# Kernel optimization log

Hardware: AMD Instinct MI355X
Metric: run time of the kernel (lower is better)

## Reference

```python
import jax, jax.numpy as jnp
import numpy as np

B, T, E, H, W = 2, 1024, 1024, 8, 31
D = 2 * W + 1  # head dim must equal 2*window_size+1 for the rel-pos broadcast


def _ln(x, w, b):
    mu = jnp.mean(x, axis=-1, keepdims=True)
    var = jnp.mean(jnp.square(x - mu), axis=-1, keepdims=True)
    return (x - mu) * jax.lax.rsqrt(var + 1e-5) * w + b


def setup_inputs() -> dict:
    key = jax.random.key(0)
    k = jax.random.split(key, 8)
    s = 0.02
    return {
        "x": jax.random.normal(k[0], (B, T, E // 2), jnp.float32),
        "ln1_w": jnp.ones(E, jnp.float32), "ln1_b": jnp.zeros(E, jnp.float32),
        "qkv_w": jax.random.normal(k[1], (3 * H * D, E), jnp.float32) * s,
        "qkv_b": jnp.zeros(3 * H * D, jnp.float32),
        "rel_pos": jax.random.normal(k[2], (D, D), jnp.float32) * s,
        "proj_w": jax.random.normal(k[3], (E, H * D), jnp.float32) * s,
        "proj_b": jnp.zeros(E, jnp.float32),
        "ln2_w": jnp.ones(E, jnp.float32), "ln2_b": jnp.zeros(E, jnp.float32),
        "fc_w": jax.random.normal(k[4], (4 * E, E), jnp.float32) * s,
        "fc_b": jnp.zeros(4 * E, jnp.float32),
        "cproj_w": jax.random.normal(k[5], (E, 4 * E), jnp.float32) * s,
        "cproj_b": jnp.zeros(E, jnp.float32),
    }


def reference(x, ln1_w, ln1_b, qkv_w, qkv_b, rel_pos, proj_w, proj_b,
              ln2_w, ln2_b, fc_w, fc_b, cproj_w, cproj_b):
    # --- RotaryEmbedding: angle = x * inv_freq; out = cat(sin, cos) -> [B,T,E]
    dim = 2 * x.shape[-1]
    inv_freq = 1.0 / 10000.0 ** (jnp.arange(0, dim, 2, dtype=jnp.float32) / dim)
    ang = x * inv_freq
    xr = jnp.concatenate([jnp.sin(ang), jnp.cos(ang)], axis=-1)  # [B,T,E]

    # --- custom windowed attention on ln_1(xr)
    h = _ln(xr, ln1_w, ln1_b)
    qkv = h @ qkv_w.T + qkv_b                       # [B,T,3*H*D]
    q, k, v = jnp.split(qkv, 3, axis=-1)

    def heads(t):
        return t.reshape(B, T, H, D).transpose(0, 2, 1, 3)  # [B,H,T,D]

    q, k, v = heads(q), heads(k), heads(v)
    # per-token q-outer-k scores (einsum '...bd,...bv->...bdv'): [B,H,T,D,D]
    scores = jnp.einsum('bhtd,bhtv->bhtdv', q, k)
    # rel-pos bias: Embedding lookup at offsets -W..W (negative indices wrap)
    bias = rel_pos[jnp.arange(-W, W + 1) % D]       # [D, D] == [2W+1, d_model]
    attn = jax.nn.softmax(scores + bias, axis=-2)   # softmax over non-canonical axis
    out = jnp.einsum('bhtdv,bhtv->bhtd', attn, v)   # apply per-token attn matrix to v
    out = out.transpose(0, 2, 1, 3).reshape(B, T, H * D)
    xa = xr + out @ proj_w.T + proj_b               # residual

    # --- MLP
    h2 = _ln(xa, ln2_w, ln2_b)
    m = jax.nn.gelu(h2 @ fc_w.T + fc_b, approximate=False) @ cproj_w.T + cproj_b
    return xa + m
```

## Files before the change

### kernel.cpp

```cpp
#include <hip/hip_runtime.h>
#include <hip/hip_bf16.h>


typedef __bf16 bf16;
typedef bf16 bf16x8 __attribute__((ext_vector_type(8)));
typedef bf16 bf16x4 __attribute__((ext_vector_type(4)));
typedef bf16 bf16x2 __attribute__((ext_vector_type(2)));
typedef float f32x4 __attribute__((ext_vector_type(4)));

__device__ __forceinline__ float rdlane(float x, int l)
{
    return __int_as_float(__builtin_amdgcn_readlane(__float_as_int(x), l));
}

__global__ __launch_bounds__(256) void rotary_ln_kernel(
    const float* __restrict__ x, const float* __restrict__ w,
    const float* __restrict__ b, float* __restrict__ xr, bf16* __restrict__ Y)
{
    const int row = blockIdx.x;
    const int tid = threadIdx.x;
    float2 xv = *(const float2*)(x + (size_t)row * 512 + tid * 2);
    float i0 = exp2f(-(float)(2*tid)     * 0.025952563241307518f);
    float i1 = exp2f(-(float)(2*tid + 1) * 0.025952563241307518f);
    float a0 = xv.x * i0, a1 = xv.y * i1;
    float s0 = sinf(a0), s1 = sinf(a1);
    float c0 = cosf(a0), c1 = cosf(a1);
    *(float2*)(xr + (size_t)row * 1024 + tid*2)       = make_float2(s0, s1);
    *(float2*)(xr + (size_t)row * 1024 + 512 + tid*2) = make_float2(c0, c1);
    float s  = s0 + s1 + c0 + c1;
    float ss = s0*s0 + s1*s1 + c0*c0 + c1*c1;
    #pragma unroll
    for (int off = 32; off > 0; off >>= 1) {
        s  += __shfl_down(s, off);
        ss += __shfl_down(ss, off);
    }
    __shared__ float rs[4], rss[4];
    int wave = tid >> 6, lane = tid & 63;
    if (lane == 0) { rs[wave] = s; rss[wave] = ss; }
    __syncthreads();
    s  = rs[0] + rs[1] + rs[2] + rs[3];
    ss = rss[0] + rss[1] + rss[2] + rss[3];
    float mu   = s * (1.f / 1024.f);
    float var  = ss * (1.f / 1024.f) - mu * mu;
    float rstd = rsqrtf(var + 1e-5f);
    float2 w0 = *(const float2*)(w + tid*2);
    float2 b0 = *(const float2*)(b + tid*2);
    float2 w1 = *(const float2*)(w + 512 + tid*2);
    float2 b1 = *(const float2*)(b + 512 + tid*2);
    bf16x2 y0, y1;
    y0[0] = (bf16)((s0 - mu) * rstd * w0.x + b0.x);
    y0[1] = (bf16)((s1 - mu) * rstd * w0.y + b0.y);
    y1[0] = (bf16)((c0 - mu) * rstd * w1.x + b1.x);
    y1[1] = (bf16)((c1 - mu) * rstd * w1.y + b1.y);
    *(bf16x2*)(Y + (size_t)row * 1024 + tid*2)       = y0;
    *(bf16x2*)(Y + (size_t)row * 1024 + 512 + tid*2) = y1;
}

__device__ __forceinline__ void conv_chunk(
    const float* __restrict__ src, bf16* __restrict__ dst,
    int ci, int N, int K, int Kp)
{
    int kpc = Kp >> 3;
    int r  = ci / kpc;
    int kc = (ci - r * kpc) << 3;
    bf16x8 o;
    if (r < N && kc < K) {
        float4 f0 = *(const float4*)(src + (size_t)r * K + kc);
        float4 f1 = *(const float4*)(src + (size_t)r * K + kc + 4);
        o[0]=(bf16)f0.x; o[1]=(bf16)f0.y; o[2]=(bf16)f0.z; o[3]=(bf16)f0.w;
        o[4]=(bf16)f1.x; o[5]=(bf16)f1.y; o[6]=(bf16)f1.z; o[7]=(bf16)f1.w;
    } else {
        #pragma unroll
        for (int j = 0; j < 8; ++j) o[j] = (bf16)0.f;
    }
    *(bf16x8*)(dst + (size_t)r * Kp + kc) = o;
}

__global__ __launch_bounds__(256) void conv_all_kernel(
    const float* __restrict__ qkv_w, const float* __restrict__ proj_w,
    const float* __restrict__ fc_w,  const float* __restrict__ cproj_w,
    const float* __restrict__ qkv_b,
    bf16* __restrict__ wqkv, bf16* __restrict__ wproj,
    bf16* __restrict__ wfc,  bf16* __restrict__ wcproj,
    float* __restrict__ qkvb_p)
{
    if (blockIdx.x == 5120) {
        for (int i = threadIdx.x; i < 1536; i += 256)
            qkvb_p[i] = (i < 1512) ? qkv_b[i] : 0.f;
        return;
    }
    int idx = blockIdx.x * 256 + threadIdx.x;
    if      (idx < 196608)  conv_chunk(qkv_w,   wqkv,   idx,          1512, 1024, 1024);
    else if (idx < 262144)  conv_chunk(proj_w,  wproj,  idx - 196608, 1024,  504,  512);
    else if (idx < 786432)  conv_chunk(fc_w,    wfc,    idx - 262144, 4096, 1024, 1024);
    else                    conv_chunk(cproj_w, wcproj, idx - 786432, 1024, 4096, 4096);
}

__device__ __forceinline__ void gload16(const char* src, char* ldsdst)
{
    __builtin_amdgcn_global_load_lds(
        (const __attribute__((address_space(1))) void*)src,
        (__attribute__((address_space(3))) void*)ldsdst, 16, 0, 0);
}
__device__ __forceinline__ float gelu_exact(float v)
{
    return 0.5f * v * (1.f + erff(v * 0.70710678118654752f));
}

template<int EPI>
__global__ __launch_bounds__(256, 4) void gemm6_kernel(
    const bf16* __restrict__ A, const bf16* __restrict__ Wt,
    const float* __restrict__ bias, bf16* __restrict__ Cb,
    int N, int Kp, int ksplit)
{
    __shared__ __align__(16) char lds[2][12288];

    const int tid  = threadIdx.x;
    const int w    = tid >> 6;
    const int lane = tid & 63;

    const int gx = gridDim.x, gy = gridDim.y;
    const int nwg = gx * gy * gridDim.z;
    const int chunk = nwg >> 3;
    int id = (blockIdx.z * gy + blockIdx.y) * gx + blockIdx.x;
    int sw = (id & 7) * chunk + (id >> 3);
    const int bx = sw % gx;
    const int t2 = sw / gx;
    const int by = t2 % gy;
    const int bz = t2 / gy;

    const int row0 = by * 64;
    const int col0 = bx * 128;
    const int wr = (w >> 1) * 32;
    const int wc = (w & 1) * 64;
    const int rl = lane & 15;
    const int kb16 = (lane >> 4) * 16;

    const size_t strideBy = (size_t)Kp * 2;
    const size_t kz = (size_t)bz * ksplit * 2;
    const char* Abase = (const char*)A  + (size_t)row0 * strideBy + kz;
    const char* Wbase = (const char*)Wt + (size_t)col0 * strideBy + kz;

    const size_t srcA0 = (size_t)(tid >> 2) * strideBy + (tid & 3) * 16;
    size_t srcB[2];
    #pragma unroll
    for (int i = 0; i < 2; ++i) {
        int o = (i * 256 + tid) * 16;
        srcB[i] = (size_t)(o >> 6) * strideBy + (o & 63);
    }

    f32x4 acc[2][4] = {};

    auto STAGE = [&](int buf, int kt) {
        const char* ab = Abase + (size_t)kt * 64;
        const char* wb = Wbase + (size_t)kt * 64;
        gload16(ab + srcA0, &lds[buf][0] + tid * 16);
        #pragma unroll
        for (int i = 0; i < 2; ++i)
            gload16(wb + srcB[i], &lds[buf][4096] + (i * 256 + tid) * 16);
    };

    const int niter = ksplit >> 5;
    STAGE(0, 0);
    __syncthreads();
    for (int kt = 0; kt < niter; ++kt) {
        if (kt + 1 < niter)
            STAGE((kt + 1) & 1, kt + 1);
        const char* base = lds[kt & 1];
        bf16x8 af[2], bfr[4];
        #pragma unroll
        for (int mi = 0; mi < 2; ++mi)
            af[mi] = *(const bf16x8*)(base + ((wr + mi*16 + rl) << 6) + kb16);
        #pragma unroll
        for (int nj = 0; nj < 4; ++nj)
            bfr[nj] = *(const bf16x8*)(base + 4096 + ((wc + nj*16 + rl) << 6) + kb16);
        __builtin_amdgcn_s_setprio(1);
        #pragma unroll
        for (int mi = 0; mi < 2; ++mi)
            #pragma unroll
            for (int nj = 0; nj < 4; ++nj)
                acc[mi][nj] = __builtin_amdgcn_mfma_f32_16x16x32_bf16(
                    af[mi], bfr[nj], acc[mi][nj], 0, 0, 0);
        __builtin_amdgcn_s_setprio(0);
        __syncthreads();
    }

    const int rq = (lane >> 4) * 4;
    bf16* Cbz = Cb;
    if (EPI == 3) Cbz += (size_t)bz * 2048 * N;
    #pragma unroll
    for (int mi = 0; mi < 2; ++mi) {
        #pragma unroll
        for (int rj = 0; rj < 4; ++rj) {
            int row = row0 + wr + mi*16 + rq + rj;
            #pragma unroll
            for (int nj = 0; nj < 4; ++nj) {
                int col = col0 + wc + nj*16 + rl;
                float c = acc[mi][nj][rj];
                size_t off = (size_t)row * N + col;
                if (EPI == 0)      Cbz[off] = (bf16)(c + bias[col]);
                else if (EPI == 1) Cbz[off] = (bf16)gelu_exact(c + bias[col]);
                else               Cbz[off] = (bf16)c;
            }
        }
    }
}

template<int P>
__global__ __launch_bounds__(256) void reduce_kernel(
    const bf16* __restrict__ parts, const float* __restrict__ bias,
    const float* R, float* out)
{
    int row = blockIdx.x;
    int c = threadIdx.x * 4;
    size_t off = (size_t)row * 1024 + c;
    float4 bv = *(const float4*)(bias + c);
    float4 o = *(const float4*)(R + off);
    o.x += bv.x; o.y += bv.y; o.z += bv.z; o.w += bv.w;
    #pragma unroll
    for (int p = 0; p < P; ++p) {
        bf16x4 v = *(const bf16x4*)(parts + (size_t)p * 2048 * 1024 + off);
        o.x += (float)v[0]; o.y += (float)v[1];
        o.z += (float)v[2]; o.w += (float)v[3];
    }
    *(float4*)(out + off) = o;
}

__global__ __launch_bounds__(256) void reduceln_kernel(
    const bf16* __restrict__ parts, const float* __restrict__ bias,
    const float* __restrict__ R, const float* __restrict__ lnw,
    const float* __restrict__ lnb, float* __restrict__ out,
    bf16* __restrict__ Y)
{
    int row = blockIdx.x;
    int c = threadIdx.x * 4;
    size_t off = (size_t)row * 1024 + c;
    float4 bv = *(const float4*)(bias + c);
    float4 o  = *(const float4*)(R + off);
    o.x += bv.x; o.y += bv.y; o.z += bv.z; o.w += bv.w;
    #pragma unroll
    for (int p = 0; p < 2; ++p) {
        bf16x4 v = *(const bf16x4*)(parts + (size_t)p * 2048 * 1024 + off);
        o.x += (float)v[0]; o.y += (float)v[1];
        o.z += (float)v[2]; o.w += (float)v[3];
    }
    *(float4*)(out + off) = o;
    float s  = o.x + o.y + o.z + o.w;
    float ss = o.x*o.x + o.y*o.y + o.z*o.z + o.w*o.w;
    #pragma unroll
    for (int of = 32; of > 0; of >>= 1) {
        s  += __shfl_down(s, of);
        ss += __shfl_down(ss, of);
    }
    __shared__ float rs[4], rss[4];
    int wave = threadIdx.x >> 6, lane = threadIdx.x & 63;
    if (lane == 0) { rs[wave] = s; rss[wave] = ss; }
    __syncthreads();
    s  = rs[0] + rs[1] + rs[2] + rs[3];
    ss = rss[0] + rss[1] + rss[2] + rss[3];
    float mu  = s * (1.f / 1024.f);
    float var = ss * (1.f / 1024.f) - mu * mu;
    float rstd = rsqrtf(var + 1e-5f);
    float4 wv = *(const float4*)(lnw + c);
    float4 lb = *(const float4*)(lnb + c);
    bf16 y[4];
    y[0] = (bf16)((o.x - mu) * rstd * wv.x + lb.x);
    y[1] = (bf16)((o.y - mu) * rstd * wv.y + lb.y);
    y[2] = (bf16)((o.z - mu) * rstd * wv.z + lb.z);
    y[3] = (bf16)((o.w - mu) * rstd * wv.w + lb.w);
    *(uint2*)(Y + (size_t)row * 1024 + c) = *(uint2*)y;
}

__global__ __launch_bounds__(1024) void attn3_kernel(
    const bf16* __restrict__ qkv, const float* __restrict__ rel_pos,
    bf16* __restrict__ outp)
{
    __shared__ float bR[4096];
    __shared__ float bT[4096];
    for (int i = threadIdx.x; i < 4096; i += 1024) {
        int d = i >> 6, v = i & 63;
        float val = (d < 63 && v < 63)
                  ? rel_pos[((d + 32) % 63) * 63 + v] * 1.4426950408889634f
                  : -1e30f;
        bR[(d << 6) + (((v >> 2) ^ (d & 15)) << 2) + (v & 3)] = val;
        bT[(v << 6) + (((d >> 2) ^ (v & 15)) << 2) + (d & 3)] = val;
    }
    __syncthreads();

    const int wave = threadIdx.x >> 6;
    const int lane = threadIdx.x & 63;
    const int tk  = blockIdx.x * 16 + wave;
    const int row = tk >> 3;
    const int h   = tk & 7;
    const bf16* base = qkv + (size_t)row * 1536 + h * 63;
    float q_own = 0.f, k_own = 0.f, v_own = 0.f;
    if (lane < 63) {
        q_own = (float)base[lane] * 1.4426950408889634f;
        k_own = (float)base[504 + lane];
        v_own = (float)base[1008 + lane];
    }

    const float* myT = bT + (lane << 6);
    const int sw = lane & 15;
    float z0 = 0.f, z1 = 0.f, z2 = 0.f, z3 = 0.f;
    #pragma unroll
    for (int g = 0; g < 16; ++g) {
        f32x4 bb = *(const f32x4*)(myT + ((g ^ sw) << 2));
        z0 += __builtin_amdgcn_exp2f(fmaf(rdlane(q_own, 4*g + 0), k_own, bb[0]));
        z1 += __builtin_amdgcn_exp2f(fmaf(rdlane(q_own, 4*g + 1), k_own, bb[1]));
        z2 += __builtin_amdgcn_exp2f(fmaf(rdlane(q_own, 4*g + 2), k_own, bb[2]));
        z3 += __builtin_amdgcn_exp2f(fmaf(rdlane(q_own, 4*g + 3), k_own, bb[3]));
    }
    float Z = (z0 + z1) + (z2 + z3);
    float w_own = (lane < 63) ? v_own / Z : 0.f;

    const float* myR = bR + (lane << 6);
    float a0 = 0.f, a1 = 0.f, a2 = 0.f, a3 = 0.f;
    #pragma unroll
    for (int g = 0; g < 16; ++g) {
        f32x4 bb = *(const f32x4*)(myR + ((g ^ sw) << 2));
        a0 = fmaf(__builtin_amdgcn_exp2f(fmaf(q_own, rdlane(k_own, 4*g + 0), bb[0])),
                  rdlane(w_own, 4*g + 0), a0);
        a1 = fmaf(__builtin_amdgcn_exp2f(fmaf(q_own, rdlane(k_own, 4*g + 1), bb[1])),
                  rdlane(w_own, 4*g + 1), a1);
        a2 = fmaf(__builtin_amdgcn_exp2f(fmaf(q_own, rdlane(k_own, 4*g + 2), bb[2])),
                  rdlane(w_own, 4*g + 2), a2);
        a3 = fmaf(__builtin_amdgcn_exp2f(fmaf(q_own, rdlane(k_own, 4*g + 3), bb[3])),
                  rdlane(w_own, 4*g + 3), a3);
    }
    float acc = (a0 + a1) + (a2 + a3);

    if (lane < 63)
        outp[(size_t)row * 512 + h*63 + lane] = (bf16)acc;
    if (h == 7 && lane == 63) {
        #pragma unroll
        for (int j = 0; j < 8; ++j)
            outp[(size_t)row * 512 + 504 + j] = (bf16)0.f;
    }
}

extern "C" void kernel_launch(void* const* d_in, const int* in_sizes, int n_in,
                              void* d_out, int out_size, void* d_ws, size_t ws_size,
                              hipStream_t stream)
{
    const float* x       = (const float*)d_in[0];
    const float* ln1_w   = (const float*)d_in[1];
    const float* ln1_b   = (const float*)d_in[2];
    const float* qkv_w   = (const float*)d_in[3];
    const float* qkv_b   = (const float*)d_in[4];
    const float* rel_pos = (const float*)d_in[5];
    const float* proj_w  = (const float*)d_in[6];
    const float* proj_b  = (const float*)d_in[7];
    const float* ln2_w   = (const float*)d_in[8];
    const float* ln2_b   = (const float*)d_in[9];
    const float* fc_w    = (const float*)d_in[10];
    const float* fc_b    = (const float*)d_in[11];
    const float* cproj_w = (const float*)d_in[12];
    const float* cproj_b = (const float*)d_in[13];
    float* out = (float*)d_out;

    char* p = (char*)d_ws;
    float* xr      = (float*)p;            p += (size_t)2048*1024*4;
    bf16*  h_bf    = (bf16*)p;             p += (size_t)2048*1024*2;
    bf16*  wqkv    = (bf16*)p;             p += (size_t)1536*1024*2;
    bf16*  wproj   = (bf16*)p;             p += (size_t)1024*512*2;
    bf16*  wfc     = (bf16*)p;             p += (size_t)4096*1024*2;
    bf16*  wcproj  = (bf16*)p;             p += (size_t)1024*4096*2;
    float* qkvb_p  = (float*)p;            p += 8192;
    bf16*  attn_bf = (bf16*)p;             p += (size_t)2048*512*2;
    bf16*  qkvb    = (bf16*)p;
    bf16*  fc_act  = (bf16*)p;
    bf16*  proj_part = qkvb;
    bf16*  cp_part = (bf16*)d_ws;

    conv_all_kernel<<<5121, 256, 0, stream>>>(qkv_w, proj_w, fc_w, cproj_w, qkv_b,
                                              wqkv, wproj, wfc, wcproj, qkvb_p);
    rotary_ln_kernel<<<2048, 256, 0, stream>>>(x, ln1_w, ln1_b, xr, h_bf);
    gemm6_kernel<0><<<dim3(12,32,1), 256, 0, stream>>>(h_bf, wqkv, qkvb_p,
                                                       qkvb, 1536, 1024, 1024);
    attn3_kernel<<<1024, 1024, 0, stream>>>(qkvb, rel_pos, attn_bf);
    gemm6_kernel<3><<<dim3(8,32,2), 256, 0, stream>>>(attn_bf, wproj, nullptr,
                                                      proj_part, 1024, 512, 256);
    reduceln_kernel<<<2048, 256, 0, stream>>>(proj_part, proj_b, xr,
                                              ln2_w, ln2_b, out, h_bf);
    gemm6_kernel<1><<<dim3(32,32,1), 256, 0, stream>>>(h_bf, wfc, fc_b,
                                                       fc_act, 4096, 1024, 1024);
    gemm6_kernel<3><<<dim3(8,32,4), 256, 0, stream>>>(fc_act, wcproj, nullptr,
                                                      cp_part, 1024, 4096, 1024);
    reduce_kernel<4><<<2048, 256, 0, stream>>>(cp_part, cproj_b, out, out);
}
```

Before: 144.5 us.

## Triple-buffer GEMM LDS staging with XOR swizzle and explicit waitcnt barriers

The GEMM kernel moves from double to triple buffering in LDS, prefetching two K-tiles ahead. __syncthreads is replaced by explicit vmcnt/lgkmcnt waits plus s_barrier, so global-to-LDS loads can stay in flight across iterations. An XOR swizzle on the 16-byte slots of each 64-byte row is applied to both the direct-to-LDS loads and the fragment reads, aimed at reducing LDS bank conflicts. This raises LDS use to 36KB per block, which may limit occupancy at 4 blocks per CU, and the hand-coded wait counts must match the exact number of issued loads.

New measurement: 149.4 us. 1.03x slower.

```diff
diff --git a/kernel.cpp b/kernel.cpp
--- a/kernel.cpp
+++ b/kernel.cpp
@@ -96,6 +96,19 @@
     else                    conv_chunk(cproj_w, wcproj, idx - 786432, 1024, 4096, 4096);
 }
 
+template<int N> __device__ __forceinline__ void vmwait()
+{
+    if constexpr      (N==0) asm volatile("s_waitcnt vmcnt(0)" ::: "memory");
+    else if constexpr (N==3) asm volatile("s_waitcnt vmcnt(3)" ::: "memory");
+}
+__device__ __forceinline__ void lgkmwait0()
+{
+    asm volatile("s_waitcnt lgkmcnt(0)" ::: "memory");
+}
+__device__ __forceinline__ void hw_barrier()
+{
+    asm volatile("s_barrier" ::: "memory");
+}
 __device__ __forceinline__ void gload16(const char* src, char* ldsdst)
 {
     __builtin_amdgcn_global_load_lds(
@@ -108,12 +121,12 @@
 }
 
 template<int EPI>
-__global__ __launch_bounds__(256, 4) void gemm6_kernel(
+__global__ __launch_bounds__(256, 4) void gemm7_kernel(
     const bf16* __restrict__ A, const bf16* __restrict__ Wt,
     const float* __restrict__ bias, bf16* __restrict__ Cb,
     int N, int Kp, int ksplit)
 {
-    __shared__ __align__(16) char lds[2][12288];
+    __shared__ __align__(16) char lds[3][12288];
 
     const int tid  = threadIdx.x;
     const int w    = tid >> 6;
@@ -134,19 +147,23 @@
     const int wr = (w >> 1) * 32;
     const int wc = (w & 1) * 64;
     const int rl = lane & 15;
-    const int kb16 = (lane >> 4) * 16;
+    const int slotR = lane >> 4;
 
     const size_t strideBy = (size_t)Kp * 2;
     const size_t kz = (size_t)bz * ksplit * 2;
     const char* Abase = (const char*)A  + (size_t)row0 * strideBy + kz;
     const char* Wbase = (const char*)Wt + (size_t)col0 * strideBy + kz;
 
-    const size_t srcA0 = (size_t)(tid >> 2) * strideBy + (tid & 3) * 16;
+    const int arow = tid >> 2;
+    const size_t srcA0 = (size_t)arow * strideBy
+                       + (size_t)(((tid & 3) ^ ((arow >> 1) & 3)) << 4);
     size_t srcB[2];
     #pragma unroll
     for (int i = 0; i < 2; ++i) {
         int o = (i * 256 + tid) * 16;
-        srcB[i] = (size_t)(o >> 6) * strideBy + (o & 63);
+        int r = o >> 6;
+        int s = ((o & 63) >> 4) ^ ((r >> 1) & 3);
+        srcB[i] = (size_t)r * strideBy + (size_t)(s << 4);
     }
 
     f32x4 acc[2][4] = {};
@@ -162,18 +179,27 @@
 
     const int niter = ksplit >> 5;
     STAGE(0, 0);
-    __syncthreads();
+    STAGE(1, 1);
+    vmwait<3>();
+    hw_barrier();
+
+    int cur = 0, stg = 2;
     for (int kt = 0; kt < niter; ++kt) {
-        if (kt + 1 < niter)
-            STAGE((kt + 1) & 1, kt + 1);
-        const char* base = lds[kt & 1];
+        if (kt + 2 < niter) STAGE(stg, kt + 2);
+        const char* base = lds[cur];
         bf16x8 af[2], bfr[4];
         #pragma unroll
-        for (int mi = 0; mi < 2; ++mi)
-            af[mi] = *(const bf16x8*)(base + ((wr + mi*16 + rl) << 6) + kb16);
-        #pragma unroll
-        for (int nj = 0; nj < 4; ++nj)
-            bfr[nj] = *(const bf16x8*)(base + 4096 + ((wc + nj*16 + rl) << 6) + kb16);
+        for (int mi = 0; mi < 2; ++mi) {
+            int r = wr + mi * 16 + rl;
+            af[mi] = *(const bf16x8*)
+                (base + (r << 6) + ((slotR ^ ((r >> 1) & 3)) << 4));
+        }
+        #pragma unroll
+        for (int nj = 0; nj < 4; ++nj) {
+            int r = wc + nj * 16 + rl;
+            bfr[nj] = *(const bf16x8*)
+                (base + 4096 + (r << 6) + ((slotR ^ ((r >> 1) & 3)) << 4));
+        }
         __builtin_amdgcn_s_setprio(1);
         #pragma unroll
         for (int mi = 0; mi < 2; ++mi)
@@ -182,7 +208,15 @@
                 acc[mi][nj] = __builtin_amdgcn_mfma_f32_16x16x32_bf16(
                     af[mi], bfr[nj], acc[mi][nj], 0, 0, 0);
         __builtin_amdgcn_s_setprio(0);
-        __syncthreads();
+
+        if (kt + 1 < niter) {
+            lgkmwait0();
+            if (kt + 2 < niter) vmwait<3>();
+            else                vmwait<0>();
+            hw_barrier();
+        }
+        cur = (cur == 2) ? 0 : cur + 1;
+        stg = (stg == 2) ? 0 : stg + 1;
     }
 
     const int rq = (lane >> 4) * 4;
@@ -376,16 +410,16 @@
     conv_all_kernel<<<5121, 256, 0, stream>>>(qkv_w, proj_w, fc_w, cproj_w, qkv_b,
                                               wqkv, wproj, wfc, wcproj, qkvb_p);
     rotary_ln_kernel<<<2048, 256, 0, stream>>>(x, ln1_w, ln1_b, xr, h_bf);
-    gemm6_kernel<0><<<dim3(12,32,1), 256, 0, stream>>>(h_bf, wqkv, qkvb_p,
+    gemm7_kernel<0><<<dim3(12,32,1), 256, 0, stream>>>(h_bf, wqkv, qkvb_p,
                                                        qkvb, 1536, 1024, 1024);
     attn3_kernel<<<1024, 1024, 0, stream>>>(qkvb, rel_pos, attn_bf);
-    gemm6_kernel<3><<<dim3(8,32,2), 256, 0, stream>>>(attn_bf, wproj, nullptr,
+    gemm7_kernel<3><<<dim3(8,32,2), 256, 0, stream>>>(attn_bf, wproj, nullptr,
                                                       proj_part, 1024, 512, 256);
     reduceln_kernel<<<2048, 256, 0, stream>>>(proj_part, proj_b, xr,
                                               ln2_w, ln2_b, out, h_bf);
-    gemm6_kernel<1><<<dim3(32,32,1), 256, 0, stream>>>(h_bf, wfc, fc_b,
+    gemm7_kernel<1><<<dim3(32,32,1), 256, 0, stream>>>(h_bf, wfc, fc_b,
                                                        fc_act, 4096, 1024, 1024);
-    gemm6_kernel<3><<<dim3(8,32,4), 256, 0, stream>>>(fc_act, wcproj, nullptr,
+    gemm7_kernel<3><<<dim3(8,32,4), 256, 0, stream>>>(fc_act, wcproj, nullptr,
                                                       cp_part, 1024, 4096, 1024);
     reduce_kernel<4><<<2048, 256, 0, stream>>>(cp_part, cproj_b, out, out);
 }
```
